# Kernel tuning notes

Hardware: AMD Instinct MI355X
Metric: run time of the kernel (lower is better)

## Reference

```python
import jax, jax.numpy as jnp
import numpy as np

N = 100000      # nodes
E = 1600000     # edges
IN = 64; H = 64; OUT = 64
ED = 32         # edge_dim
L = 2           # num_layers
NT = 3          # num_node_types
ET = 4          # num_edge_types
EPS = 1e-5


def setup_inputs() -> dict:
    key = jax.random.key(0)
    ks = jax.random.split(key, 16)
    x = jax.random.normal(ks[0], (N, IN), dtype=jnp.float32)
    edge_index = jax.random.randint(ks[1], (2, E), 0, N, dtype=jnp.int64)
    edge_attr = jax.random.normal(ks[2], (E, ED), dtype=jnp.float32)
    node_type = jax.random.randint(ks[3], (N,), 0, NT, dtype=jnp.int64)
    edge_type = jax.random.randint(ks[4], (E,), 0, ET, dtype=jnp.int64)
    # parameters (stacked over layers; layer0 in_channels == hidden so shapes match)
    Wn = jax.random.normal(ks[5], (L, NT, H, H), dtype=jnp.float32) * 0.05   # per-node-type linear
    bn = jax.random.normal(ks[6], (L, NT, H), dtype=jnp.float32) * 0.05
    Wm = jax.random.normal(ks[7], (L, ET, ED), dtype=jnp.float32) * 0.1     # edge MLP Linear(ED,1)
    bm = jax.random.normal(ks[8], (L, ET), dtype=jnp.float32) * 0.1
    emb = jax.random.normal(ks[9], (L, ET, ED), dtype=jnp.float32) * 0.1    # edge_type_emb
    ln_g = jnp.ones((L, H), dtype=jnp.float32)
    ln_b = jnp.zeros((L, H), dtype=jnp.float32)
    fc_w = jax.random.normal(ks[10], (OUT, H), dtype=jnp.float32) * 0.05
    fc_b = jnp.zeros((OUT,), dtype=jnp.float32)
    return {"x": x, "edge_index": edge_index, "edge_attr": edge_attr,
            "node_type": node_type, "edge_type": edge_type,
            "Wn": Wn, "bn": bn, "Wm": Wm, "bm": bm, "emb": emb,
            "ln_g": ln_g, "ln_b": ln_b, "fc_w": fc_w, "fc_b": fc_b}


def _layernorm(h, g, b):
    mu = jnp.mean(h, axis=-1, keepdims=True)
    var = jnp.mean((h - mu) ** 2, axis=-1, keepdims=True)
    return (h - mu) * jax.lax.rsqrt(var + EPS) * g + b


def reference(x, edge_index, edge_attr, node_type, edge_type,
              Wn, bn, Wm, bm, emb, ln_g, ln_b, fc_w, fc_b):
    src = edge_index[0]  # x_j
    dst = edge_index[1]  # x_i (aggregation target)
    for l in range(L):
        # HydroConv message: softplus(edge MLP per edge type) * (x_j - x_i)
        ea = edge_attr + emb[l][edge_type]                               # [E, ED]
        w = jax.nn.softplus(jnp.einsum('ed,ed->e', ea, Wm[l][edge_type])
                            + bm[l][edge_type])                          # [E]
        msg = w[:, None] * (x[src] - x[dst])                             # [E, H]
        aggr = jax.ops.segment_sum(msg, dst, num_segments=N)            # [N, H]
        # per-node-type linear update
        h = jnp.einsum('nd,ndo->no', aggr, Wn[l][node_type]) + bn[l][node_type]
        h = jax.nn.relu(h)
        x = _layernorm(h, ln_g[l], ln_b[l])
    return x @ fc_w.T + fc_b
```

## Files before the change

### kernel.cpp

```cpp
#include <hip/hip_runtime.h>

#define NN 100000
#define NE 1600000
#define HDIM 64
#define EDIM 32
#define NTT 3
#define ETT 4
#define NTILES 6250
#define LEPS 1e-5f
#define NBKT 782
#define EPB 8192
#define NWGA 196
#define SCAP 4096
#define NSC (NBKT * NWGA)
#define SBLK 150

typedef _Float16 half2v __attribute__((ext_vector_type(2)));
typedef _Float16 half4v __attribute__((ext_vector_type(4)));
typedef _Float16 half8v __attribute__((ext_vector_type(8)));
typedef float f32x4 __attribute__((ext_vector_type(4)));

__global__ void prep_kernel(const float* __restrict__ Wn, const float* __restrict__ fc_w,
                            _Float16* __restrict__ Wp, _Float16* __restrict__ fcp) {
    const int i = blockIdx.x * blockDim.x + threadIdx.x;
    if (i < 6 * HDIM * HDIM) {
        const int lt = i >> 12;
        const int o = (i >> 6) & 63;
        const int d = i & 63;
        Wp[i] = (_Float16)Wn[((size_t)lt * 64 + d) * 64 + o];
    } else if (i < 6 * HDIM * HDIM + HDIM * HDIM) {
        const int j = i - 6 * HDIM * HDIM;
        fcp[j] = (_Float16)fc_w[j];
    }
}

__global__ __launch_bounds__(256) void edge_weights_kernel(
        const float* __restrict__ edge_attr,
        const int* __restrict__ eisrc,
        const int* __restrict__ edge_type,
        const float* __restrict__ Wm,
        const float* __restrict__ bm,
        const float* __restrict__ emb,
        int2* __restrict__ ewu) {
    __shared__ float sWm[2 * ETT * EDIM];
    __shared__ float sc[2 * ETT];
    const int tid = threadIdx.x;
    if (tid < 2 * ETT * EDIM) sWm[tid] = Wm[tid];
    __syncthreads();
    if (tid < 2 * ETT) {
        float c = bm[tid];
        #pragma unroll
        for (int k = 0; k < EDIM; k++) c += emb[tid * EDIM + k] * sWm[tid * EDIM + k];
        sc[tid] = c;
    }
    __syncthreads();
    const int lane = tid & 63;
    const int wv = tid >> 6;
    const int sub = lane >> 3;
    const int k = lane & 7;
    const int ebase = blockIdx.x * 128 + wv * 32;
    #pragma unroll
    for (int it = 0; it < 4; it++) {
        const int e = ebase + it * 8 + sub;
        const int et = edge_type[e];
        const float4 v = ((const float4*)(edge_attr + (size_t)e * EDIM))[k];
        const float4 a = ((const float4*)(sWm + et * EDIM))[k];
        const float4 b = ((const float4*)(sWm + (ETT + et) * EDIM))[k];
        float d0 = v.x * a.x + v.y * a.y + v.z * a.z + v.w * a.w;
        float d1 = v.x * b.x + v.y * b.y + v.z * b.z + v.w * b.w;
        d0 += __shfl_xor(d0, 1); d1 += __shfl_xor(d1, 1);
        d0 += __shfl_xor(d0, 2); d1 += __shfl_xor(d1, 2);
        d0 += __shfl_xor(d0, 4); d1 += __shfl_xor(d1, 4);
        if (k == 0) {
            d0 += sc[et];
            d1 += sc[ETT + et];
            const float w0 = fmaxf(d0, 0.f) + log1pf(expf(-fabsf(d0)));
            const float w1 = fmaxf(d1, 0.f) + log1pf(expf(-fabsf(d1)));
            union { half2v h; int i; } u;
            u.h[0] = (_Float16)w0;
            u.h[1] = (_Float16)w1;
            ewu[e] = make_int2(u.i, eisrc[e]);
        }
    }
}

__global__ void xcvt_kernel(const float* __restrict__ x, _Float16* __restrict__ xs) {
    const int i = blockIdx.x * blockDim.x + threadIdx.x;
    const float4 v = ((const float4*)x)[i];
    half4v o = { (_Float16)v.x, (_Float16)v.y, (_Float16)v.z, (_Float16)v.w };
    ((half4v*)xs)[i] = o;
}

__global__ __launch_bounds__(256) void hist_kernel(const int* __restrict__ eidst,
                                                   int* __restrict__ whist) {
    __shared__ int h[NBKT];
    for (int i = threadIdx.x; i < NBKT; i += 256) h[i] = 0;
    __syncthreads();
    const int wg = blockIdx.x;
    const int start = wg * EPB, end = min(start + EPB, NE);
    for (int e = start + threadIdx.x; e < end; e += 256)
        atomicAdd(&h[eidst[e] >> 7], 1);
    __syncthreads();
    for (int i = threadIdx.x; i < NBKT; i += 256) whist[i * NWGA + wg] = h[i];
}

__global__ __launch_bounds__(256) void partial2_kernel(const int* __restrict__ in,
                                                       int* __restrict__ psum) {
    __shared__ int red[256];
    const int b = blockIdx.x, t = threadIdx.x;
    const int base = b * 1024 + t * 4;
    int s = 0;
    #pragma unroll
    for (int k = 0; k < 4; k++) { const int i = base + k; if (i < NSC) s += in[i]; }
    red[t] = s;
    __syncthreads();
    for (int d = 128; d > 0; d >>= 1) {
        if (t < d) red[t] += red[t + d];
        __syncthreads();
    }
    if (t == 0) psum[b] = red[0];
}

__global__ void bscan2_kernel(const int* __restrict__ psum, int* __restrict__ poff) {
    __shared__ int v[256];
    const int t = threadIdx.x;
    v[t] = (t < SBLK) ? psum[t] : 0;
    __syncthreads();
    for (int d = 1; d < 256; d <<= 1) {
        const int x = (t >= d) ? v[t - d] : 0;
        __syncthreads();
        v[t] += x;
        __syncthreads();
    }
    poff[t] = (t == 0) ? 0 : v[t - 1];
}

__global__ __launch_bounds__(256) void wscan2_kernel(const int* __restrict__ in,
                                                     const int* __restrict__ poff,
                                                     int* __restrict__ out) {
    __shared__ int red[256];
    const int b = blockIdx.x, t = threadIdx.x;
    const int base = b * 1024 + t * 4;
    int d4[4];
    #pragma unroll
    for (int k = 0; k < 4; k++) d4[k] = (base + k < NSC) ? in[base + k] : 0;
    const int s = d4[0] + d4[1] + d4[2] + d4[3];
    red[t] = s;
    __syncthreads();
    for (int d = 1; d < 256; d <<= 1) {
        const int x = (t >= d) ? red[t - d] : 0;
        __syncthreads();
        red[t] += x;
        __syncthreads();
    }
    int run = poff[b] + ((t == 0) ? 0 : red[t - 1]);
    #pragma unroll
    for (int k = 0; k < 4; k++) {
        if (base + k < NSC) { out[base + k] = run; run += d4[k]; }
    }
}

__global__ __launch_bounds__(256) void binb_kernel(const int2* __restrict__ ewu,
                                                   const int* __restrict__ eidst,
                                                   const int* __restrict__ wscan,
                                                   int2* __restrict__ brec) {
    __shared__ int lcur[NBKT];
    const int wg = blockIdx.x;
    for (int i = threadIdx.x; i < NBKT; i += 256) lcur[i] = wscan[i * NWGA + wg];
    __syncthreads();
    const int start = wg * EPB, end = min(start + EPB, NE);
    for (int e = start + threadIdx.x; e < end; e += 256) {
        const int dst = eidst[e];
        const int2 r = ewu[e];
        const int pos = atomicAdd(&lcur[dst >> 7], 1);
        brec[pos] = make_int2(r.x, r.y | ((dst & 127) << 17));
    }
}

__global__ __launch_bounds__(256) void sortb_kernel(const int2* __restrict__ brec,
                                                    const int* __restrict__ wscan,
                                                    int* __restrict__ off,
                                                    int2* __restrict__ ews) {
    __shared__ int hist[128];
    __shared__ int excl[128];
    __shared__ int2 sorted[SCAP];
    const int b = blockIdx.x;
    const int node0 = b << 7;
    const int nn = min(128, NN - node0);
    const int base = wscan[b * NWGA];
    const int end = (b < NBKT - 1) ? wscan[(b + 1) * NWGA] : NE;
    const int n = end - base;
    const int t = threadIdx.x;
    if (t < 128) hist[t] = 0;
    __syncthreads();
    for (int i = t; i < n; i += 256)
        atomicAdd(&hist[(brec[base + i].y >> 17) & 127], 1);
    __syncthreads();
    if (t < 128) excl[t] = hist[t];
    __syncthreads();
    for (int d = 1; d < 128; d <<= 1) {
        int v = 0;
        if (t < 128 && t >= d) v = excl[t - d];
        __syncthreads();
        if (t < 128) excl[t] += v;
        __syncthreads();
    }
    if (t < 128) {
        const int ex = excl[t] - hist[t];
        if (t < nn) off[node0 + t] = base + ex;
        hist[t] = ex;
    }
    if (b == NBKT - 1 && t == 0) off[NN] = NE;
    __syncthreads();
    for (int i = t; i < n; i += 256) {
        const int2 r = brec[base + i];
        const int dstl = (r.y >> 17) & 127;
        const int2 o = make_int2(r.x, r.y & 0x1FFFF);
        const int pos = atomicAdd(&hist[dstl], 1);
        if (pos < SCAP) sorted[pos] = o;
        else ews[base + pos] = o;
    }
    __syncthreads();
    const int m = min(n, SCAP);
    for (int i = t; i < m; i += 256) ews[base + i] = sorted[i];
}

#define ROWS16(OFS)                                                        \
    _Pragma("unroll")                                                      \
    for (int g = 0; g < 4; g++) {                                          \
        const int r = (OFS) + g * 4 + sub;                                 \
        const float w = __shfl(rw, r);                                     \
        const int s = __shfl(rs, r);                                       \
        const half4v xv = *(const half4v*)(xs + (size_t)s * HDIM + fl * 4);\
        a0 += w * (float)xv[0]; a1 += w * (float)xv[1];                    \
        a2 += w * (float)xv[2]; a3 += w * (float)xv[3];                    \
        sw += w;                                                           \
    }

template<int LAYER>
__global__ __launch_bounds__(256) void gather_kernel(
        const _Float16* __restrict__ xs,
        const int2* __restrict__ ew,
        const int* __restrict__ off,
        _Float16* __restrict__ aggr) {
    const int lane = threadIdx.x & 63;
    const int wid = threadIdx.x >> 6;
    const int p = blockIdx.x * 4 + wid;
    const int sub = lane >> 4;
    const int fl = lane & 15;
    const int lo = off[p], hi = off[p + 1];
    const int deg = hi - lo;
    const half4v xt = *(const half4v*)(xs + (size_t)p * HDIM + fl * 4);

    const int cl = max(hi - 1, 0);
    const int2 rec = ew[min(lo + lane, cl)];
    union { int i; half2v h; } u; u.i = rec.x;
    float rw = (lo + lane < hi) ? (float)u.h[LAYER] : 0.f;
    int rs = rec.y;

    float a0 = 0.f, a1 = 0.f, a2 = 0.f, a3 = 0.f, sw = 0.f;
    if (deg <= 16) {
        ROWS16(0)
    } else if (deg <= 32) {
        ROWS16(0) ROWS16(16)
    } else {
        ROWS16(0) ROWS16(16) ROWS16(32) ROWS16(48)
        for (int base = lo + 64; base < hi; base += 64) {
            const int2 rec2 = ew[min(base + lane, cl)];
            union { int i; half2v h; } u2; u2.i = rec2.x;
            rw = (base + lane < hi) ? (float)u2.h[LAYER] : 0.f;
            rs = rec2.y;
            ROWS16(0) ROWS16(16) ROWS16(32) ROWS16(48)
        }
    }

    a0 += __shfl_xor(a0, 16); a1 += __shfl_xor(a1, 16);
    a2 += __shfl_xor(a2, 16); a3 += __shfl_xor(a3, 16);
    sw += __shfl_xor(sw, 16);
    a0 += __shfl_xor(a0, 32); a1 += __shfl_xor(a1, 32);
    a2 += __shfl_xor(a2, 32); a3 += __shfl_xor(a3, 32);
    sw += __shfl_xor(sw, 32);
    if (sub == 0) {
        half4v o;
        o[0] = (_Float16)(a0 - sw * (float)xt[0]);
        o[1] = (_Float16)(a1 - sw * (float)xt[1]);
        o[2] = (_Float16)(a2 - sw * (float)xt[2]);
        o[3] = (_Float16)(a3 - sw * (float)xt[3]);
        *(half4v*)(aggr + (size_t)p * HDIM + fl * 4) = o;
    }
}

template<int FUSE>
__global__ __launch_bounds__(256) void update_kernel(const _Float16* __restrict__ aggr,
                                                     const int* __restrict__ ntype,
                                                     const _Float16* __restrict__ Wp,
                                                     const float* __restrict__ bnp,
                                                     const float* __restrict__ lng,
                                                     const float* __restrict__ lnb,
                                                     const _Float16* __restrict__ fcp,
                                                     const float* __restrict__ fcb,
                                                     _Float16* __restrict__ xout,
                                                     float* __restrict__ fout) {
    __shared__ float scst[320];
    __shared__ f32x4 sraw[4 * 4608 / 16];
    for (int i = threadIdx.x; i < 320; i += 256)
        scst[i] = (i < 192) ? bnp[i] : ((i < 256) ? lng[i - 192] : lnb[i - 256]);
    __syncthreads();

    const int wid = threadIdx.x >> 6;
    const int lane = threadIdx.x & 63;
    const int tile = blockIdx.x * 4 + wid;
    if (tile >= NTILES) return;
    const int fl = lane & 15;
    const int gq = lane >> 4;
    const size_t R = (size_t)tile * 16;

    const half8v A0 = *(const half8v*)(aggr + (R + fl) * HDIM + gq * 8);
    const half8v A1 = *(const half8v*)(aggr + (R + fl) * HDIM + 32 + gq * 8);
    int nt[4];
    #pragma unroll
    for (int r = 0; r < 4; r++) nt[r] = ntype[R + gq * 4 + r];

    float h[4][4];
    #pragma unroll
    for (int ob = 0; ob < 4; ob++) {
        const int col = ob * 16 + fl;
        f32x4 c[3];
        #pragma unroll
        for (int t = 0; t < 3; t++) {
            const half8v B0 = *(const half8v*)(Wp + t * 4096 + col * 64 + gq * 8);
            const half8v B1 = *(const half8v*)(Wp + t * 4096 + col * 64 + 32 + gq * 8);
            f32x4 z = { 0.f, 0.f, 0.f, 0.f };
            z = __builtin_amdgcn_mfma_f32_16x16x32_f16(A0, B0, z, 0, 0, 0);
            z = __builtin_amdgcn_mfma_f32_16x16x32_f16(A1, B1, z, 0, 0, 0);
            c[t] = z;
        }
        #pragma unroll
        for (int r = 0; r < 4; r++) {
            float v = (nt[r] == 0) ? c[0][r] : ((nt[r] == 1) ? c[1][r] : c[2][r]);
            v += scst[nt[r] * 64 + col];
            h[ob][r] = fmaxf(v, 0.f);
        }
    }

    float mu[4], rs[4];
    #pragma unroll
    for (int r = 0; r < 4; r++) {
        float m = h[0][r] + h[1][r] + h[2][r] + h[3][r];
        m += __shfl_xor(m, 1); m += __shfl_xor(m, 2);
        m += __shfl_xor(m, 4); m += __shfl_xor(m, 8);
        mu[r] = m * (1.f / 64.f);
        const float d0 = h[0][r] - mu[r], d1 = h[1][r] - mu[r];
        const float d2 = h[2][r] - mu[r], d3 = h[3][r] - mu[r];
        float v = d0 * d0 + d1 * d1 + d2 * d2 + d3 * d3;
        v += __shfl_xor(v, 1); v += __shfl_xor(v, 2);
        v += __shfl_xor(v, 4); v += __shfl_xor(v, 8);
        rs[r] = rsqrtf(v * (1.f / 64.f) + LEPS);
    }

    _Float16* wb = (_Float16*)sraw + (size_t)wid * 2304;
    #pragma unroll
    for (int ob = 0; ob < 4; ob++) {
        const int col = ob * 16 + fl;
        const float gg = scst[192 + col], bb = scst[256 + col];
        #pragma unroll
        for (int r = 0; r < 4; r++) {
            const float xn = (h[ob][r] - mu[r]) * rs[r] * gg + bb;
            wb[(gq * 4 + r) * 72 + col] = (_Float16)xn;
        }
    }
    __threadfence_block();

    if (!FUSE) {
        const int rr = lane >> 2, cg = lane & 3;
        const half8v o0 = *(const half8v*)(wb + rr * 72 + cg * 16);
        const half8v o1 = *(const half8v*)(wb + rr * 72 + cg * 16 + 8);
        *(half8v*)(xout + (R + rr) * HDIM + cg * 16) = o0;
        *(half8v*)(xout + (R + rr) * HDIM + cg * 16 + 8) = o1;
    } else {
        const half8v FA0 = *(const half8v*)(wb + fl * 72 + gq * 8);
        const half8v FA1 = *(const half8v*)(wb + fl * 72 + 32 + gq * 8);
        float fo[4][4];
        #pragma unroll
        for (int ob = 0; ob < 4; ob++) {
            const int col = ob * 16 + fl;
            const half8v FB0 = *(const half8v*)(fcp + col * 64 + gq * 8);
            const half8v FB1 = *(const half8v*)(fcp + col * 64 + 32 + gq * 8);
            f32x4 z = { 0.f, 0.f, 0.f, 0.f };
            z = __builtin_amdgcn_mfma_f32_16x16x32_f16(FA0, FB0, z, 0, 0, 0);
            z = __builtin_amdgcn_mfma_f32_16x16x32_f16(FA1, FB1, z, 0, 0, 0);
            const float fb = fcb[col];
            #pragma unroll
            for (int r = 0; r < 4; r++) fo[ob][r] = z[r] + fb;
        }
        __threadfence_block();
        float* fb32 = (float*)((char*)sraw + (size_t)wid * 4608);
        #pragma unroll
        for (int ob = 0; ob < 4; ob++) {
            const int col = ob * 16 + fl;
            #pragma unroll
            for (int r = 0; r < 4; r++) fb32[(gq * 4 + r) * 68 + col] = fo[ob][r];
        }
        __threadfence_block();
        #pragma unroll
        for (int rr = 0; rr < 16; rr++)
            fout[(R + rr) * HDIM + lane] = fb32[rr * 68 + lane];
    }
}

extern "C" void kernel_launch(void* const* d_in, const int* in_sizes, int n_in,
                              void* d_out, int out_size, void* d_ws, size_t ws_size,
                              hipStream_t stream) {
    const float* x         = (const float*)d_in[0];
    const int*   ei        = (const int*)d_in[1];
    const float* edge_attr = (const float*)d_in[2];
    const int*   node_type = (const int*)d_in[3];
    const int*   edge_type = (const int*)d_in[4];
    const float* Wn        = (const float*)d_in[5];
    const float* bn        = (const float*)d_in[6];
    const float* Wm        = (const float*)d_in[7];
    const float* bm        = (const float*)d_in[8];
    const float* emb       = (const float*)d_in[9];
    const float* ln_g      = (const float*)d_in[10];
    const float* ln_b      = (const float*)d_in[11];
    const float* fc_w      = (const float*)d_in[12];
    const float* fc_b      = (const float*)d_in[13];
    float* out = (float*)d_out;

    char* W = (char*)d_ws;
    int2*      ewu  = (int2*)W;
    int2*      ews  = (int2*)(W + 12800000);
    _Float16*  xs   = (_Float16*)(W + 25600000);
    _Float16*  x1s  = (_Float16*)(W + 38400000);
    int2*      brec = (int2*)(W + 51200000);
    _Float16*  aggr = (_Float16*)brec;
    char*      p3   = W + 64000000;
    _Float16*  Wp   = (_Float16*)p3;
    _Float16*  fcp  = (_Float16*)(p3 + 49152);
    int*       off  = (int*)(p3 + 49152 + 8192);
    int*       psum2 = off + NN + 16;
    int*       poff2 = psum2 + 256;
    int*       whist = poff2 + 256;
    int*       wscan = whist + NSC;

    prep_kernel<<<112, 256, 0, stream>>>(Wn, fc_w, Wp, fcp);
    edge_weights_kernel<<<NE / 128, 256, 0, stream>>>(edge_attr, ei, edge_type,
                                                      Wm, bm, emb, ewu);
    xcvt_kernel<<<6250, 256, 0, stream>>>(x, xs);

    hist_kernel<<<NWGA, 256, 0, stream>>>(ei + NE, whist);
    partial2_kernel<<<SBLK, 256, 0, stream>>>(whist, psum2);
    bscan2_kernel<<<1, 256, 0, stream>>>(psum2, poff2);
    wscan2_kernel<<<SBLK, 256, 0, stream>>>(whist, poff2, wscan);
    binb_kernel<<<NWGA, 256, 0, stream>>>(ewu, ei + NE, wscan, brec);
    sortb_kernel<<<NBKT, 256, 0, stream>>>(brec, wscan, off, ews);

    gather_kernel<0><<<NN / 4, 256, 0, stream>>>(xs, ews, off, aggr);
    update_kernel<0><<<(NTILES + 3) / 4, 256, 0, stream>>>(aggr, node_type,
        Wp, bn, ln_g, ln_b, fcp, fc_b, x1s, nullptr);
    gather_kernel<1><<<NN / 4, 256, 0, stream>>>(x1s, ews, off, aggr);
    update_kernel<1><<<(NTILES + 3) / 4, 256, 0, stream>>>(aggr, node_type,
        Wp + 3 * 4096, bn + NTT * HDIM, ln_g + HDIM, ln_b + HDIM, fcp, fc_b, nullptr, out);
}
```

Before: 268.8 us.

## Process two destination nodes per wavefront in gather and widen binning grid

The gather kernel now has each wavefront handle two consecutive destination nodes, interleaving their 16-row chunks so more independent loads are in flight, and it launches half as many blocks. Separately, the edge binning pass uses smaller per-workgroup chunks (more workgroups), which enlarges the histogram and scan arrays, so the block-level scan moves to 1024 threads. The node interleaving aims to hide gather latency for low-degree nodes at the cost of more registers and divergence when the two degrees differ. The binning change trades more parallelism in hist/binb for a bigger scan.

```diff
diff --git a/kernel.cpp b/kernel.cpp
--- a/kernel.cpp
+++ b/kernel.cpp
@@ -9,11 +9,11 @@
 #define NTILES 6250
 #define LEPS 1e-5f
 #define NBKT 782
-#define EPB 8192
-#define NWGA 196
+#define EPB 2048
+#define NWGA 782
 #define SCAP 4096
 #define NSC (NBKT * NWGA)
-#define SBLK 150
+#define SBLK 598
 
 typedef _Float16 half2v __attribute__((ext_vector_type(2)));
 typedef _Float16 half4v __attribute__((ext_vector_type(4)));
@@ -121,18 +121,19 @@
     if (t == 0) psum[b] = red[0];
 }
 
-__global__ void bscan2_kernel(const int* __restrict__ psum, int* __restrict__ poff) {
-    __shared__ int v[256];
+__global__ __launch_bounds__(1024) void bscan2_kernel(const int* __restrict__ psum,
+                                                      int* __restrict__ poff) {
+    __shared__ int v[1024];
     const int t = threadIdx.x;
     v[t] = (t < SBLK) ? psum[t] : 0;
     __syncthreads();
-    for (int d = 1; d < 256; d <<= 1) {
+    for (int d = 1; d < 1024; d <<= 1) {
         const int x = (t >= d) ? v[t - d] : 0;
         __syncthreads();
         v[t] += x;
         __syncthreads();
     }
-    poff[t] = (t == 0) ? 0 : v[t - 1];
+    if (t < SBLK) poff[t] = (t == 0) ? 0 : v[t - 1];
 }
 
 __global__ __launch_bounds__(256) void wscan2_kernel(const int* __restrict__ in,
@@ -225,16 +226,16 @@
     for (int i = t; i < m; i += 256) ews[base + i] = sorted[i];
 }
 
-#define ROWS16(OFS)                                                        \
-    _Pragma("unroll")                                                      \
-    for (int g = 0; g < 4; g++) {                                          \
-        const int r = (OFS) + g * 4 + sub;                                 \
-        const float w = __shfl(rw, r);                                     \
-        const int s = __shfl(rs, r);                                       \
-        const half4v xv = *(const half4v*)(xs + (size_t)s * HDIM + fl * 4);\
-        a0 += w * (float)xv[0]; a1 += w * (float)xv[1];                    \
-        a2 += w * (float)xv[2]; a3 += w * (float)xv[3];                    \
-        sw += w;                                                           \
+#define ROWS16G(RW, RS, A0, A1, A2, A3, SW, OFS)                            \
+    _Pragma("unroll")                                                       \
+    for (int g = 0; g < 4; g++) {                                           \
+        const int r = (OFS) + g * 4 + sub;                                  \
+        const float w = __shfl(RW, r);                                      \
+        const int s = __shfl(RS, r);                                        \
+        const half4v xv = *(const half4v*)(xs + (size_t)s * HDIM + fl * 4); \
+        A0 += w * (float)xv[0]; A1 += w * (float)xv[1];                     \
+        A2 += w * (float)xv[2]; A3 += w * (float)xv[3];                     \
+        SW += w;                                                            \
     }
 
 template<int LAYER>
@@ -245,48 +246,81 @@
         _Float16* __restrict__ aggr) {
     const int lane = threadIdx.x & 63;
     const int wid = threadIdx.x >> 6;
-    const int p = blockIdx.x * 4 + wid;
+    const int pA = (blockIdx.x * 4 + wid) * 2;
+    const int pB = pA + 1;
     const int sub = lane >> 4;
     const int fl = lane & 15;
-    const int lo = off[p], hi = off[p + 1];
-    const int deg = hi - lo;
-    const half4v xt = *(const half4v*)(xs + (size_t)p * HDIM + fl * 4);
-
-    const int cl = max(hi - 1, 0);
-    const int2 rec = ew[min(lo + lane, cl)];
-    union { int i; half2v h; } u; u.i = rec.x;
-    float rw = (lo + lane < hi) ? (float)u.h[LAYER] : 0.f;
-    int rs = rec.y;
-
-    float a0 = 0.f, a1 = 0.f, a2 = 0.f, a3 = 0.f, sw = 0.f;
-    if (deg <= 16) {
-        ROWS16(0)
-    } else if (deg <= 32) {
-        ROWS16(0) ROWS16(16)
-    } else {
-        ROWS16(0) ROWS16(16) ROWS16(32) ROWS16(48)
-        for (int base = lo + 64; base < hi; base += 64) {
-            const int2 rec2 = ew[min(base + lane, cl)];
-            union { int i; half2v h; } u2; u2.i = rec2.x;
-            rw = (base + lane < hi) ? (float)u2.h[LAYER] : 0.f;
-            rs = rec2.y;
-            ROWS16(0) ROWS16(16) ROWS16(32) ROWS16(48)
-        }
-    }
-
-    a0 += __shfl_xor(a0, 16); a1 += __shfl_xor(a1, 16);
-    a2 += __shfl_xor(a2, 16); a3 += __shfl_xor(a3, 16);
-    sw += __shfl_xor(sw, 16);
-    a0 += __shfl_xor(a0, 32); a1 += __shfl_xor(a1, 32);
-    a2 += __shfl_xor(a2, 32); a3 += __shfl_xor(a3, 32);
-    sw += __shfl_xor(sw, 32);
+    const int loA = off[pA], loB = off[pB], hiB = off[pB + 1];
+    const int hiA = loB;
+    const half4v xtA = *(const half4v*)(xs + (size_t)pA * HDIM + fl * 4);
+    const half4v xtB = *(const half4v*)(xs + (size_t)pB * HDIM + fl * 4);
+
+    const int2 recA = ew[min(loA + lane, max(hiA - 1, 0))];
+    const int2 recB = ew[min(loB + lane, max(hiB - 1, 0))];
+    union { int i; half2v h; } uA, uB;
+    uA.i = recA.x; uB.i = recB.x;
+    const float rwA = (loA + lane < hiA) ? (float)uA.h[LAYER] : 0.f;
+    const float rwB = (loB + lane < hiB) ? (float)uB.h[LAYER] : 0.f;
+    const int rsA = recA.y, rsB = recB.y;
+
+    float aA0 = 0.f, aA1 = 0.f, aA2 = 0.f, aA3 = 0.f, swA = 0.f;
+    float aB0 = 0.f, aB1 = 0.f, aB2 = 0.f, aB3 = 0.f, swB = 0.f;
+    const int cA = min((hiA - loA + 15) >> 4, 4);
+    const int cB = min((hiB - loB + 15) >> 4, 4);
+    const int cmax = max(cA, cB);
+    for (int c = 0; c < cmax; c++) {
+        const int ofs = c * 16;
+        if (c < cA) { ROWS16G(rwA, rsA, aA0, aA1, aA2, aA3, swA, ofs) }
+        if (c < cB) { ROWS16G(rwB, rsB, aB0, aB1, aB2, aB3, swB, ofs) }
+    }
+    for (int base = loA + 64; base < hiA; base += 64) {
+        const int2 r2 = ew[min(base + lane, hiA - 1)];
+        union { int i; half2v h; } u2; u2.i = r2.x;
+        const float rw2 = (base + lane < hiA) ? (float)u2.h[LAYER] : 0.f;
+        const int rs2 = r2.y;
+        ROWS16G(rw2, rs2, aA0, aA1, aA2, aA3, swA, 0)
+        ROWS16G(rw2, rs2, aA0, aA1, aA2, aA3, swA, 16)
+        ROWS16G(rw2, rs2, aA0, aA1, aA2, aA3, swA, 32)
+        ROWS16G(rw2, rs2, aA0, aA1, aA2, aA3, swA, 48)
+    }
+    for (int base = loB + 64; base < hiB; base += 64) {
+        const int2 r2 = ew[min(base + lane, hiB - 1)];
+        union { int i; half2v h; } u2; u2.i = r2.x;
+        const float rw2 = (base + lane < hiB) ? (float)u2.h[LAYER] : 0.f;
+        const int rs2 = r2.y;
+        ROWS16G(rw2, rs2, aB0, aB1, aB2, aB3, swB, 0)
+        ROWS16G(rw2, rs2, aB0, aB1, aB2, aB3, swB, 16)
+        ROWS16G(rw2, rs2, aB0, aB1, aB2, aB3, swB, 32)
+        ROWS16G(rw2, rs2, aB0, aB1, aB2, aB3, swB, 48)
+    }
+
+    aA0 += __shfl_xor(aA0, 16); aA1 += __shfl_xor(aA1, 16);
+    aA2 += __shfl_xor(aA2, 16); aA3 += __shfl_xor(aA3, 16);
+    swA += __shfl_xor(swA, 16);
+    aA0 += __shfl_xor(aA0, 32); aA1 += __shfl_xor(aA1, 32);
+    aA2 += __shfl_xor(aA2, 32); aA3 += __shfl_xor(aA3, 32);
+    swA += __shfl_xor(swA, 32);
+    aB0 += __shfl_xor(aB0, 16); aB1 += __shfl_xor(aB1, 16);
+    aB2 += __shfl_xor(aB2, 16); aB3 += __shfl_xor(aB3, 16);
+    swB += __shfl_xor(swB, 16);
+    aB0 += __shfl_xor(aB0, 32); aB1 += __shfl_xor(aB1, 32);
+    aB2 += __shfl_xor(aB2, 32); aB3 += __shfl_xor(aB3, 32);
+    swB += __shfl_xor(swB, 32);
+
     if (sub == 0) {
         half4v o;
-        o[0] = (_Float16)(a0 - sw * (float)xt[0]);
-        o[1] = (_Float16)(a1 - sw * (float)xt[1]);
-        o[2] = (_Float16)(a2 - sw * (float)xt[2]);
-        o[3] = (_Float16)(a3 - sw * (float)xt[3]);
-        *(half4v*)(aggr + (size_t)p * HDIM + fl * 4) = o;
+        o[0] = (_Float16)(aA0 - swA * (float)xtA[0]);
+        o[1] = (_Float16)(aA1 - swA * (float)xtA[1]);
+        o[2] = (_Float16)(aA2 - swA * (float)xtA[2]);
+        o[3] = (_Float16)(aA3 - swA * (float)xtA[3]);
+        *(half4v*)(aggr + (size_t)pA * HDIM + fl * 4) = o;
+    } else if (sub == 1) {
+        half4v o;
+        o[0] = (_Float16)(aB0 - swB * (float)xtB[0]);
+        o[1] = (_Float16)(aB1 - swB * (float)xtB[1]);
+        o[2] = (_Float16)(aB2 - swB * (float)xtB[2]);
+        o[3] = (_Float16)(aB3 - swB * (float)xtB[3]);
+        *(half4v*)(aggr + (size_t)pB * HDIM + fl * 4) = o;
     }
 }
 
@@ -439,8 +473,8 @@
     _Float16*  fcp  = (_Float16*)(p3 + 49152);
     int*       off  = (int*)(p3 + 49152 + 8192);
     int*       psum2 = off + NN + 16;
-    int*       poff2 = psum2 + 256;
-    int*       whist = poff2 + 256;
+    int*       poff2 = psum2 + 1024;
+    int*       whist = poff2 + 1024;
     int*       wscan = whist + NSC;
 
     prep_kernel<<<112, 256, 0, stream>>>(Wn, fc_w, Wp, fcp);
@@ -450,15 +484,15 @@
 
     hist_kernel<<<NWGA, 256, 0, stream>>>(ei + NE, whist);
     partial2_kernel<<<SBLK, 256, 0, stream>>>(whist, psum2);
-    bscan2_kernel<<<1, 256, 0, stream>>>(psum2, poff2);
+    bscan2_kernel<<<1, 1024, 0, stream>>>(psum2, poff2);
     wscan2_kernel<<<SBLK, 256, 0, stream>>>(whist, poff2, wscan);
     binb_kernel<<<NWGA, 256, 0, stream>>>(ewu, ei + NE, wscan, brec);
     sortb_kernel<<<NBKT, 256, 0, stream>>>(brec, wscan, off, ews);
 
-    gather_kernel<0><<<NN / 4, 256, 0, stream>>>(xs, ews, off, aggr);
+    gather_kernel<0><<<NN / 8, 256, 0, stream>>>(xs, ews, off, aggr);
     update_kernel<0><<<(NTILES + 3) / 4, 256, 0, stream>>>(aggr, node_type,
         Wp, bn, ln_g, ln_b, fcp, fc_b, x1s, nullptr);
-    gather_kernel<1><<<NN / 4, 256, 0, stream>>>(x1s, ews, off, aggr);
+    gather_kernel<1><<<NN / 8, 256, 0, stream>>>(x1s, ews, off, aggr);
     update_kernel<1><<<(NTILES + 3) / 4, 256, 0, stream>>>(aggr, node_type,
         Wp + 3 * 4096, bn + NTT * HDIM, ln_g + HDIM, ln_b + HDIM, fcp, fc_b, nullptr, out);
 }
```

Measured after the change: 321.9 us. 1.2x slower.

## Replace two-level workgroup-bucket scan with per-bucket totals and atomic offset claiming

Applied to the files above, without the earlier changes.

Replaces the three-kernel scan over the (bucket x workgroup) histogram with global atomic per-bucket totals computed in the histogram pass, a single 1024-thread scan over 782 bucket totals, and per-workgroup claiming of bucket slots through atomicAdd on a cursor array in the binning kernel. This removes two kernel launches and the full scan over ~153K histogram entries. In exchange, edge order within a bucket now depends on atomic claim order, so the edge order inside each node's segment can vary between runs. A memset launch and extra global atomics are added.

```diff
diff --git a/kernel.cpp b/kernel.cpp
--- a/kernel.cpp
+++ b/kernel.cpp
@@ -12,8 +12,6 @@
 #define EPB 8192
 #define NWGA 196
 #define SCAP 4096
-#define NSC (NBKT * NWGA)
-#define SBLK 150
 
 typedef _Float16 half2v __attribute__((ext_vector_type(2)));
 typedef _Float16 half4v __attribute__((ext_vector_type(4)));
@@ -92,7 +90,8 @@
 }
 
 __global__ __launch_bounds__(256) void hist_kernel(const int* __restrict__ eidst,
-                                                   int* __restrict__ whist) {
+                                                   int* __restrict__ whist,
+                                                   int* __restrict__ btot) {
     __shared__ int h[NBKT];
     for (int i = threadIdx.x; i < NBKT; i += 256) h[i] = 0;
     __syncthreads();
@@ -101,84 +100,57 @@
     for (int e = start + threadIdx.x; e < end; e += 256)
         atomicAdd(&h[eidst[e] >> 7], 1);
     __syncthreads();
-    for (int i = threadIdx.x; i < NBKT; i += 256) whist[i * NWGA + wg] = h[i];
-}
-
-__global__ __launch_bounds__(256) void partial2_kernel(const int* __restrict__ in,
-                                                       int* __restrict__ psum) {
-    __shared__ int red[256];
-    const int b = blockIdx.x, t = threadIdx.x;
-    const int base = b * 1024 + t * 4;
-    int s = 0;
-    #pragma unroll
-    for (int k = 0; k < 4; k++) { const int i = base + k; if (i < NSC) s += in[i]; }
-    red[t] = s;
-    __syncthreads();
-    for (int d = 128; d > 0; d >>= 1) {
-        if (t < d) red[t] += red[t + d];
-        __syncthreads();
-    }
-    if (t == 0) psum[b] = red[0];
-}
-
-__global__ void bscan2_kernel(const int* __restrict__ psum, int* __restrict__ poff) {
-    __shared__ int v[256];
+    for (int i = threadIdx.x; i < NBKT; i += 256) {
+        const int v = h[i];
+        whist[wg * NBKT + i] = v;
+        if (v) atomicAdd(&btot[i], v);
+    }
+}
+
+__global__ __launch_bounds__(1024) void bbase_kernel(const int* __restrict__ btot,
+                                                     int* __restrict__ bbase,
+                                                     int* __restrict__ bcur) {
+    __shared__ int v[1024];
     const int t = threadIdx.x;
-    v[t] = (t < SBLK) ? psum[t] : 0;
-    __syncthreads();
-    for (int d = 1; d < 256; d <<= 1) {
+    v[t] = (t < NBKT) ? btot[t] : 0;
+    __syncthreads();
+    for (int d = 1; d < 1024; d <<= 1) {
         const int x = (t >= d) ? v[t - d] : 0;
         __syncthreads();
         v[t] += x;
         __syncthreads();
     }
-    poff[t] = (t == 0) ? 0 : v[t - 1];
-}
-
-__global__ __launch_bounds__(256) void wscan2_kernel(const int* __restrict__ in,
-                                                     const int* __restrict__ poff,
-                                                     int* __restrict__ out) {
-    __shared__ int red[256];
-    const int b = blockIdx.x, t = threadIdx.x;
-    const int base = b * 1024 + t * 4;
-    int d4[4];
-    #pragma unroll
-    for (int k = 0; k < 4; k++) d4[k] = (base + k < NSC) ? in[base + k] : 0;
-    const int s = d4[0] + d4[1] + d4[2] + d4[3];
-    red[t] = s;
-    __syncthreads();
-    for (int d = 1; d < 256; d <<= 1) {
-        const int x = (t >= d) ? red[t - d] : 0;
-        __syncthreads();
-        red[t] += x;
-        __syncthreads();
-    }
-    int run = poff[b] + ((t == 0) ? 0 : red[t - 1]);
-    #pragma unroll
-    for (int k = 0; k < 4; k++) {
-        if (base + k < NSC) { out[base + k] = run; run += d4[k]; }
-    }
+    if (t < NBKT) {
+        const int b = (t == 0) ? 0 : v[t - 1];
+        bbase[t] = b;
+        bcur[t] = b;
+    }
+    if (t == NBKT) bbase[NBKT] = v[NBKT - 1];
 }
 
 __global__ __launch_bounds__(256) void binb_kernel(const int2* __restrict__ ewu,
                                                    const int* __restrict__ eidst,
-                                                   const int* __restrict__ wscan,
+                                                   const int* __restrict__ whist,
+                                                   int* __restrict__ bcur,
                                                    int2* __restrict__ brec) {
-    __shared__ int lcur[NBKT];
+    __shared__ int lofs[NBKT];
     const int wg = blockIdx.x;
-    for (int i = threadIdx.x; i < NBKT; i += 256) lcur[i] = wscan[i * NWGA + wg];
+    for (int i = threadIdx.x; i < NBKT; i += 256) {
+        const int h = whist[wg * NBKT + i];
+        lofs[i] = h ? atomicAdd(&bcur[i], h) : 0;
+    }
     __syncthreads();
     const int start = wg * EPB, end = min(start + EPB, NE);
     for (int e = start + threadIdx.x; e < end; e += 256) {
         const int dst = eidst[e];
         const int2 r = ewu[e];
-        const int pos = atomicAdd(&lcur[dst >> 7], 1);
+        const int pos = atomicAdd(&lofs[dst >> 7], 1);
         brec[pos] = make_int2(r.x, r.y | ((dst & 127) << 17));
     }
 }
 
 __global__ __launch_bounds__(256) void sortb_kernel(const int2* __restrict__ brec,
-                                                    const int* __restrict__ wscan,
+                                                    const int* __restrict__ bbase,
                                                     int* __restrict__ off,
                                                     int2* __restrict__ ews) {
     __shared__ int hist[128];
@@ -187,9 +159,8 @@
     const int b = blockIdx.x;
     const int node0 = b << 7;
     const int nn = min(128, NN - node0);
-    const int base = wscan[b * NWGA];
-    const int end = (b < NBKT - 1) ? wscan[(b + 1) * NWGA] : NE;
-    const int n = end - base;
+    const int base = bbase[b];
+    const int n = bbase[b + 1] - base;
     const int t = threadIdx.x;
     if (t < 128) hist[t] = 0;
     __syncthreads();
@@ -438,22 +409,21 @@
     _Float16*  Wp   = (_Float16*)p3;
     _Float16*  fcp  = (_Float16*)(p3 + 49152);
     int*       off  = (int*)(p3 + 49152 + 8192);
-    int*       psum2 = off + NN + 16;
-    int*       poff2 = psum2 + 256;
-    int*       whist = poff2 + 256;
-    int*       wscan = whist + NSC;
+    int*       btot = off + NN + 16;
+    int*       bbase = btot + NBKT;
+    int*       bcur = bbase + NBKT + 1;
+    int*       whist = bcur + NBKT;
 
     prep_kernel<<<112, 256, 0, stream>>>(Wn, fc_w, Wp, fcp);
     edge_weights_kernel<<<NE / 128, 256, 0, stream>>>(edge_attr, ei, edge_type,
                                                       Wm, bm, emb, ewu);
     xcvt_kernel<<<6250, 256, 0, stream>>>(x, xs);
 
-    hist_kernel<<<NWGA, 256, 0, stream>>>(ei + NE, whist);
-    partial2_kernel<<<SBLK, 256, 0, stream>>>(whist, psum2);
-    bscan2_kernel<<<1, 256, 0, stream>>>(psum2, poff2);
-    wscan2_kernel<<<SBLK, 256, 0, stream>>>(whist, poff2, wscan);
-    binb_kernel<<<NWGA, 256, 0, stream>>>(ewu, ei + NE, wscan, brec);
-    sortb_kernel<<<NBKT, 256, 0, stream>>>(brec, wscan, off, ews);
+    hipMemsetAsync(btot, 0, NBKT * sizeof(int), stream);
+    hist_kernel<<<NWGA, 256, 0, stream>>>(ei + NE, whist, btot);
+    bbase_kernel<<<1, 1024, 0, stream>>>(btot, bbase, bcur);
+    binb_kernel<<<NWGA, 256, 0, stream>>>(ewu, ei + NE, whist, bcur, brec);
+    sortb_kernel<<<NBKT, 256, 0, stream>>>(brec, bbase, off, ews);
 
     gather_kernel<0><<<NN / 4, 256, 0, stream>>>(xs, ews, off, aggr);
     update_kernel<0><<<(NTILES + 3) / 4, 256, 0, stream>>>(aggr, node_type,
```

Measured after the change: 276.0 us. 1.03x slower.

## Slice node features into 16-wide column planes mapped per XCD for gather locality

Applied to the files above, without the earlier changes.

Node features are stored as four column slices of 16 halves each (slice-major layout) instead of row-major 64-wide rows. The gather kernel launches four times as many blocks and maps each slice to a pair of XCDs via the block index, so each XCD's L2 only has to hold a quarter of the feature table. Each wave handles 8 edges per step with 2 features per lane, and edge and offset loads use nontemporal hints. The cost is re-reading the edge lists and offsets four times and making narrower 4-byte feature loads.

```diff
diff --git a/kernel.cpp b/kernel.cpp
--- a/kernel.cpp
+++ b/kernel.cpp
@@ -84,11 +84,18 @@
     }
 }
 
-__global__ void xcvt_kernel(const float* __restrict__ x, _Float16* __restrict__ xs) {
-    const int i = blockIdx.x * blockDim.x + threadIdx.x;
-    const float4 v = ((const float4*)x)[i];
-    half4v o = { (_Float16)v.x, (_Float16)v.y, (_Float16)v.z, (_Float16)v.w };
-    ((half4v*)xs)[i] = o;
+__global__ __launch_bounds__(256) void xcvt_kernel(const float* __restrict__ x,
+                                                   _Float16* __restrict__ xsl) {
+    const int i = blockIdx.x * 256 + threadIdx.x;
+    const float4 v0 = ((const float4*)x)[i * 2];
+    const float4 v1 = ((const float4*)x)[i * 2 + 1];
+    half8v o = { (_Float16)v0.x, (_Float16)v0.y, (_Float16)v0.z, (_Float16)v0.w,
+                 (_Float16)v1.x, (_Float16)v1.y, (_Float16)v1.z, (_Float16)v1.w };
+    const int n = i >> 3;
+    const int f0 = (i & 7) * 8;
+    const int slice = f0 >> 4;
+    const int w16 = f0 & 15;
+    *(half8v*)(xsl + ((size_t)slice * NN + n) * 16 + w16) = o;
 }
 
 __global__ __launch_bounds__(256) void hist_kernel(const int* __restrict__ eidst,
@@ -225,68 +232,69 @@
     for (int i = t; i < m; i += 256) ews[base + i] = sorted[i];
 }
 
-#define ROWS16(OFS)                                                        \
-    _Pragma("unroll")                                                      \
-    for (int g = 0; g < 4; g++) {                                          \
-        const int r = (OFS) + g * 4 + sub;                                 \
-        const float w = __shfl(rw, r);                                     \
-        const int s = __shfl(rs, r);                                       \
-        const half4v xv = *(const half4v*)(xs + (size_t)s * HDIM + fl * 4);\
-        a0 += w * (float)xv[0]; a1 += w * (float)xv[1];                    \
-        a2 += w * (float)xv[2]; a3 += w * (float)xv[3];                    \
-        sw += w;                                                           \
+#define ROW8(OFS)                                                           \
+    {                                                                       \
+        const int r_ = (OFS) + sub;                                         \
+        const float w_ = __shfl(rw, r_);                                    \
+        const int s_ = __shfl(rs, r_);                                      \
+        const half2v xv_ = *(const half2v*)(xp + (size_t)s_ * 16 + fl * 2); \
+        a0 += w_ * (float)xv_[0];                                           \
+        a1 += w_ * (float)xv_[1];                                           \
+        sw += w_;                                                           \
     }
 
 template<int LAYER>
 __global__ __launch_bounds__(256) void gather_kernel(
-        const _Float16* __restrict__ xs,
+        const _Float16* __restrict__ xsl,
         const int2* __restrict__ ew,
         const int* __restrict__ off,
         _Float16* __restrict__ aggr) {
+    const int bi = blockIdx.x;
+    const int xcd = bi & 7;
+    const int slice = xcd >> 1;
+    const int grp = (bi >> 3) * 2 + (xcd & 1);
+    const int wid = threadIdx.x >> 6;
     const int lane = threadIdx.x & 63;
-    const int wid = threadIdx.x >> 6;
-    const int p = blockIdx.x * 4 + wid;
-    const int sub = lane >> 4;
-    const int fl = lane & 15;
-    const int lo = off[p], hi = off[p + 1];
+    const int p = grp * 4 + wid;
+    const int sub = lane >> 3;
+    const int fl = lane & 7;
+    const _Float16* xp = xsl + (size_t)slice * NN * 16;
+
+    const int lo = __builtin_nontemporal_load(off + p);
+    const int hi = __builtin_nontemporal_load(off + p + 1);
     const int deg = hi - lo;
-    const half4v xt = *(const half4v*)(xs + (size_t)p * HDIM + fl * 4);
+    const half2v xt = *(const half2v*)(xp + (size_t)p * 16 + fl * 2);
 
     const int cl = max(hi - 1, 0);
-    const int2 rec = ew[min(lo + lane, cl)];
-    union { int i; half2v h; } u; u.i = rec.x;
+    long long rr = __builtin_nontemporal_load((const long long*)(ew + min(lo + lane, cl)));
+    union { int i; half2v h; } u; u.i = (int)rr;
     float rw = (lo + lane < hi) ? (float)u.h[LAYER] : 0.f;
-    int rs = rec.y;
-
-    float a0 = 0.f, a1 = 0.f, a2 = 0.f, a3 = 0.f, sw = 0.f;
+    int rs = (int)(rr >> 32);
+
+    float a0 = 0.f, a1 = 0.f, sw = 0.f;
     if (deg <= 16) {
-        ROWS16(0)
+        ROW8(0) ROW8(8)
     } else if (deg <= 32) {
-        ROWS16(0) ROWS16(16)
+        ROW8(0) ROW8(8) ROW8(16) ROW8(24)
     } else {
-        ROWS16(0) ROWS16(16) ROWS16(32) ROWS16(48)
+        ROW8(0) ROW8(8) ROW8(16) ROW8(24) ROW8(32) ROW8(40) ROW8(48) ROW8(56)
         for (int base = lo + 64; base < hi; base += 64) {
-            const int2 rec2 = ew[min(base + lane, cl)];
-            union { int i; half2v h; } u2; u2.i = rec2.x;
-            rw = (base + lane < hi) ? (float)u2.h[LAYER] : 0.f;
-            rs = rec2.y;
-            ROWS16(0) ROWS16(16) ROWS16(32) ROWS16(48)
-        }
-    }
-
-    a0 += __shfl_xor(a0, 16); a1 += __shfl_xor(a1, 16);
-    a2 += __shfl_xor(a2, 16); a3 += __shfl_xor(a3, 16);
-    sw += __shfl_xor(sw, 16);
-    a0 += __shfl_xor(a0, 32); a1 += __shfl_xor(a1, 32);
-    a2 += __shfl_xor(a2, 32); a3 += __shfl_xor(a3, 32);
-    sw += __shfl_xor(sw, 32);
+            rr = __builtin_nontemporal_load((const long long*)(ew + min(base + lane, cl)));
+            u.i = (int)rr;
+            rw = (base + lane < hi) ? (float)u.h[LAYER] : 0.f;
+            rs = (int)(rr >> 32);
+            ROW8(0) ROW8(8) ROW8(16) ROW8(24) ROW8(32) ROW8(40) ROW8(48) ROW8(56)
+        }
+    }
+
+    a0 += __shfl_xor(a0, 8);  a1 += __shfl_xor(a1, 8);  sw += __shfl_xor(sw, 8);
+    a0 += __shfl_xor(a0, 16); a1 += __shfl_xor(a1, 16); sw += __shfl_xor(sw, 16);
+    a0 += __shfl_xor(a0, 32); a1 += __shfl_xor(a1, 32); sw += __shfl_xor(sw, 32);
     if (sub == 0) {
-        half4v o;
+        half2v o;
         o[0] = (_Float16)(a0 - sw * (float)xt[0]);
         o[1] = (_Float16)(a1 - sw * (float)xt[1]);
-        o[2] = (_Float16)(a2 - sw * (float)xt[2]);
-        o[3] = (_Float16)(a3 - sw * (float)xt[3]);
-        *(half4v*)(aggr + (size_t)p * HDIM + fl * 4) = o;
+        *(half2v*)(aggr + (size_t)p * HDIM + slice * 16 + fl * 2) = o;
     }
 }
 
@@ -299,7 +307,7 @@
                                                      const float* __restrict__ lnb,
                                                      const _Float16* __restrict__ fcp,
                                                      const float* __restrict__ fcb,
-                                                     _Float16* __restrict__ xout,
+                                                     _Float16* __restrict__ xslout,
                                                      float* __restrict__ fout) {
     __shared__ float scst[320];
     __shared__ f32x4 sraw[4 * 4608 / 16];
@@ -375,8 +383,9 @@
         const int rr = lane >> 2, cg = lane & 3;
         const half8v o0 = *(const half8v*)(wb + rr * 72 + cg * 16);
         const half8v o1 = *(const half8v*)(wb + rr * 72 + cg * 16 + 8);
-        *(half8v*)(xout + (R + rr) * HDIM + cg * 16) = o0;
-        *(half8v*)(xout + (R + rr) * HDIM + cg * 16 + 8) = o1;
+        _Float16* xo = xslout + ((size_t)cg * NN + (R + rr)) * 16;
+        *(half8v*)(xo) = o0;
+        *(half8v*)(xo + 8) = o1;
     } else {
         const half8v FA0 = *(const half8v*)(wb + fl * 72 + gq * 8);
         const half8v FA1 = *(const half8v*)(wb + fl * 72 + 32 + gq * 8);
@@ -430,8 +439,8 @@
     char* W = (char*)d_ws;
     int2*      ewu  = (int2*)W;
     int2*      ews  = (int2*)(W + 12800000);
-    _Float16*  xs   = (_Float16*)(W + 25600000);
-    _Float16*  x1s  = (_Float16*)(W + 38400000);
+    _Float16*  xsl0 = (_Float16*)(W + 25600000);
+    _Float16*  xsl1 = (_Float16*)(W + 38400000);
     int2*      brec = (int2*)(W + 51200000);
     _Float16*  aggr = (_Float16*)brec;
     char*      p3   = W + 64000000;
@@ -446,7 +455,7 @@
     prep_kernel<<<112, 256, 0, stream>>>(Wn, fc_w, Wp, fcp);
     edge_weights_kernel<<<NE / 128, 256, 0, stream>>>(edge_attr, ei, edge_type,
                                                       Wm, bm, emb, ewu);
-    xcvt_kernel<<<6250, 256, 0, stream>>>(x, xs);
+    xcvt_kernel<<<NN * 8 / 256, 256, 0, stream>>>(x, xsl0);
 
     hist_kernel<<<NWGA, 256, 0, stream>>>(ei + NE, whist);
     partial2_kernel<<<SBLK, 256, 0, stream>>>(whist, psum2);
@@ -455,10 +464,10 @@
     binb_kernel<<<NWGA, 256, 0, stream>>>(ewu, ei + NE, wscan, brec);
     sortb_kernel<<<NBKT, 256, 0, stream>>>(brec, wscan, off, ews);
 
-    gather_kernel<0><<<NN / 4, 256, 0, stream>>>(xs, ews, off, aggr);
+    gather_kernel<0><<<NN, 256, 0, stream>>>(xsl0, ews, off, aggr);
     update_kernel<0><<<(NTILES + 3) / 4, 256, 0, stream>>>(aggr, node_type,
-        Wp, bn, ln_g, ln_b, fcp, fc_b, x1s, nullptr);
-    gather_kernel<1><<<NN / 4, 256, 0, stream>>>(x1s, ews, off, aggr);
+        Wp, bn, ln_g, ln_b, fcp, fc_b, xsl1, nullptr);
+    gather_kernel<1><<<NN, 256, 0, stream>>>(xsl1, ews, off, aggr);
     update_kernel<1><<<(NTILES + 3) / 4, 256, 0, stream>>>(aggr, node_type,
         Wp + 3 * 4096, bn + NTT * HDIM, ln_g + HDIM, ln_b + HDIM, fcp, fc_b, nullptr, out);
 }
```

After: 428.4 us. 1.59x slower.
